# Optimization experiments

Measured on AMD Instinct MI355X. Metric: run time of the kernel, lower is better.

Reference implementation:

```python
import jax, jax.numpy as jnp
import numpy as np

LORA_ALPHA = 32
RANK = 16
TOP_K = 2
SCALING = LORA_ALPHA / RANK  # lora_alpha / r
EPS = 1e-9


def setup_inputs() -> dict:
    key = jax.random.key(0)
    ks = jax.random.split(key, 6)
    B, S, D_IN, D_OUT, E, R = 4, 2048, 4096, 4096, 8, RANK
    x = jax.random.normal(ks[0], (B, S, D_IN), dtype=jnp.float32)
    W = jax.random.normal(ks[1], (D_OUT, D_IN), dtype=jnp.float32) * (1.0 / np.sqrt(D_IN))
    bias = jax.random.normal(ks[2], (D_OUT,), dtype=jnp.float32) * 0.02
    route_W = jax.random.normal(ks[3], (E, D_IN), dtype=jnp.float32) * (1.0 / np.sqrt(D_IN))
    lora_A = jax.random.normal(ks[4], (E, R, D_IN), dtype=jnp.float32) * (1.0 / np.sqrt(D_IN))
    lora_B = jax.random.normal(ks[5], (D_OUT, R), dtype=jnp.float32)
    lora_B = jnp.broadcast_to(lora_B, (E, D_OUT, R)) * 0.01  # small nonzero so lora path matters
    return {"x": x, "W": W, "bias": bias, "route_W": route_W,
            "lora_A": lora_A, "lora_B": jnp.asarray(lora_B)}


def reference(x, W, bias, route_W, lora_A, lora_B):
    # Base dense projection: y = x W^T + b   [B,S,out]
    base = jnp.einsum('bsi,oi->bso', x, W) + bias

    # Router: softmax over experts in fp32, then top-k gating
    gate_score = jnp.einsum('bsi,ei->bse', x, route_W)          # [B,S,E]
    probs = jax.nn.softmax(gate_score.astype(jnp.float32), axis=-1)
    topk_vals, topk_idx = jax.lax.top_k(probs, TOP_K)           # [B,S,k]
    # renorm (top_k < lora_nums)
    topk_vals = topk_vals / (jnp.sum(topk_vals, axis=-1, keepdims=True) + EPS)
    # dense routing weights: zeros with top-k values scattered back  [B,S,E]
    E = probs.shape[-1]
    routing_weight = jnp.sum(
        jax.nn.one_hot(topk_idx, E, dtype=base.dtype) * topk_vals[..., None].astype(base.dtype),
        axis=-2)

    # Expert LoRA: identical math to the gather/index_add loop, expressed as
    # a dense weighted combine (weights are exactly 0 for unrouted experts).
    xf = x.astype(jnp.float32)
    h = jnp.einsum('bsi,eri->bser', xf, lora_A.astype(jnp.float32))      # [B,S,E,r] (small)
    hw = h * routing_weight.astype(jnp.float32)[..., None]               # gate per expert
    lora_out = jnp.einsum('bser,eor->bso', hw, lora_B.astype(jnp.float32))

    result = base + lora_out.astype(base.dtype) * SCALING
    return result, routing_weight, gate_score
```

## Files before the change

### kernel.cpp

```cpp
#include <hip/hip_runtime.h>
#include <hip/hip_bf16.h>

typedef __bf16 bf16_t;
typedef __bf16 bf16x8 __attribute__((ext_vector_type(8)));
typedef float floatx4 __attribute__((ext_vector_type(4)));

#define M_TOK 8192
#define K_DIM 4096
#define N_OUT 4096
#define NEXP  8
#define LRANK 16
#define KEXT  128
#define SCALING 2.0f

#define GLOAD_LDS16(g, l) \
    __builtin_amdgcn_global_load_lds((const __attribute__((address_space(1))) void*)(g), \
                                     (__attribute__((address_space(3))) void*)(l), 16, 0, 0)


__device__ __forceinline__ void pack4(bf16_t* dst, float4 v) {
    union { bf16_t h[4]; uint2 u; } t;
    t.h[0] = (bf16_t)v.x; t.h[1] = (bf16_t)v.y;
    t.h[2] = (bf16_t)v.z; t.h[3] = (bf16_t)v.w;
    *(uint2*)dst = t.u;
}

__device__ __forceinline__ void cvt8_body(const float* __restrict__ src,
                                          bf16_t* __restrict__ dst, int blk) {
    size_t i = (size_t)blk * 256 + threadIdx.x;
    float4 a = ((const float4*)src)[i * 2];
    float4 b = ((const float4*)src)[i * 2 + 1];
    union { bf16_t h[8]; uint4 u; } t;
    t.h[0] = (bf16_t)a.x; t.h[1] = (bf16_t)a.y; t.h[2] = (bf16_t)a.z; t.h[3] = (bf16_t)a.w;
    t.h[4] = (bf16_t)b.x; t.h[5] = (bf16_t)b.y; t.h[6] = (bf16_t)b.z; t.h[7] = (bf16_t)b.w;
    ((uint4*)dst)[i] = t.u;
}


#define PREP_W_BLKS   8192
#define PREP_A_BLKS   256
#define PREP_B_BLKS   2048

__global__ __launch_bounds__(256) void prep_all(const float* __restrict__ W,
                                                const float* __restrict__ loraA,
                                                const float* __restrict__ loraB,
                                                bf16_t* __restrict__ Wb,
                                                bf16_t* __restrict__ aflat,
                                                bf16_t* __restrict__ bflat) {
    int b = blockIdx.x;
    if (b < PREP_W_BLKS) {
        cvt8_body(W, Wb, b);
    } else if (b < PREP_W_BLKS + PREP_A_BLKS) {
        cvt8_body(loraA, aflat, b - PREP_W_BLKS);
    } else {
        int g = (b - PREP_W_BLKS - PREP_A_BLKS) * 256 + threadIdx.x;
        int o = g >> 7, j = g & 127;
        int e = j >> 4, r = j & 15;
        bflat[g] = (bf16_t)loraB[((size_t)e * N_OUT + o) * LRANK + r];
    }
}


__global__ __launch_bounds__(256) void gate_cvt16(const float* __restrict__ x,
                                                  const float* __restrict__ routeW,
                                                  bf16_t* __restrict__ xb,
                                                  float* __restrict__ rw_out,
                                                  float* __restrict__ gate_out)
{
    __shared__ float rwT[NEXP][256];
    int tid = threadIdx.x, lane = tid & 63, wave = tid >> 6;
    int tl = lane >> 4, seg = lane & 15;
    int t = blockIdx.x * 16 + wave * 4 + tl;
    const float* xrow = x + (size_t)t * K_DIM;
    bf16_t* xbrow = xb + (size_t)t * K_DIM;

    float acc[NEXP];
    #pragma unroll
    for (int e = 0; e < NEXP; ++e) acc[e] = 0.f;

    int srow = tid >> 5, scol = (tid & 31) * 8;

    for (int kk = 0; kk < K_DIM / 256; ++kk) {
        {
            const float4* src = (const float4*)(routeW + (size_t)srow * K_DIM + kk * 256 + scol);
            float4 v0 = src[0], v1 = src[1];
            *(float4*)&rwT[srow][scol]     = v0;
            *(float4*)&rwT[srow][scol + 4] = v1;
        }
        __syncthreads();
        #pragma unroll
        for (int kc = 0; kc < 4; ++kc) {
            int kloc = kc * 64 + seg * 4;
            int k = kk * 256 + kloc;
            float4 xv = *(const float4*)(xrow + k);
            union { bf16_t h[4]; uint2 u; } cv;
            cv.h[0] = (bf16_t)xv.x; cv.h[1] = (bf16_t)xv.y;
            cv.h[2] = (bf16_t)xv.z; cv.h[3] = (bf16_t)xv.w;
            *(uint2*)(xbrow + k) = cv.u;
            #pragma unroll
            for (int e = 0; e < NEXP; ++e) {
                float4 wv = *(const float4*)&rwT[e][kloc];
                acc[e] += xv.x * wv.x + xv.y * wv.y + xv.z * wv.z + xv.w * wv.w;
            }
        }
        __syncthreads();
    }

    #pragma unroll
    for (int e = 0; e < NEXP; ++e) {
        acc[e] += __shfl_xor(acc[e], 1);
        acc[e] += __shfl_xor(acc[e], 2);
        acc[e] += __shfl_xor(acc[e], 4);
        acc[e] += __shfl_xor(acc[e], 8);
    }

    if (seg == 0) {
        float mx = acc[0];
        #pragma unroll
        for (int e = 1; e < NEXP; ++e) mx = fmaxf(mx, acc[e]);
        float p[NEXP], s = 0.f;
        #pragma unroll
        for (int e = 0; e < NEXP; ++e) { p[e] = expf(acc[e] - mx); s += p[e]; }
        float inv_s = 1.0f / s;
        #pragma unroll
        for (int e = 0; e < NEXP; ++e) p[e] *= inv_s;
        int i0 = 0;
        #pragma unroll
        for (int e = 1; e < NEXP; ++e) if (p[e] > p[i0]) i0 = e;
        int i1 = (i0 == 0) ? 1 : 0;
        #pragma unroll
        for (int e = 0; e < NEXP; ++e) { if (e == i0 || e == i1) continue; if (p[e] > p[i1]) i1 = e; }
        float v0 = p[i0], v1 = p[i1];
        float inv = 1.0f / (v0 + v1 + 1e-9f);
        float r[NEXP];
        #pragma unroll
        for (int e = 0; e < NEXP; ++e) r[e] = 0.f;
        r[i0] = v0 * inv; r[i1] = v1 * inv;
        #pragma unroll
        for (int e = 0; e < NEXP; ++e) {
            gate_out[(size_t)t * NEXP + e] = acc[e];
            rw_out[(size_t)t * NEXP + e]  = r[e];
        }
    }
}


__global__ __launch_bounds__(256) void h_kernel_v3(const bf16_t* __restrict__ xb,
                                                   const bf16_t* __restrict__ aflat,
                                                   const float* __restrict__ rw,
                                                   bf16_t* __restrict__ hw)
{
    __shared__ bf16_t As[4 * 32 * 32];
    __shared__ bf16_t Bs[4 * 128 * 32];
    int tid = threadIdx.x, lane = tid & 63, wave = tid >> 6;
    int lrow = lane & 15, lq = lane >> 4;
    int n0 = wave * 32;
    int m0 = blockIdx.x * 32;
    floatx4 acc[2][2] = {};

    const bf16_t* srcA[2];
    #pragma unroll
    for (int i = 0; i < 2; ++i) {
        int idx = i * 256 + tid;
        int ks = idx >> 7, r = (idx >> 2) & 31, cc2 = idx & 3;
        srcA[i] = xb + (size_t)(m0 + r) * K_DIM + ks * 32 + cc2 * 8;
    }
    const bf16_t* srcB[8];
    #pragma unroll
    for (int i = 0; i < 8; ++i) {
        int idx = i * 256 + tid;
        int ks = idx >> 9, r = (idx >> 2) & 127, cc2 = idx & 3;
        srcB[i] = aflat + (size_t)r * K_DIM + ks * 32 + cc2 * 8;
    }

    for (int k0 = 0; k0 < K_DIM; k0 += 128) {
        #pragma unroll
        for (int i = 0; i < 2; ++i)
            GLOAD_LDS16(srcA[i] + k0, (char*)As + (i * 256 + wave * 64) * 16);
        #pragma unroll
        for (int i = 0; i < 8; ++i)
            GLOAD_LDS16(srcB[i] + k0, (char*)Bs + (i * 256 + wave * 64) * 16);
        __syncthreads();
        #pragma unroll
        for (int ks = 0; ks < 4; ++ks) {
            bf16x8 af[2], bfr[2];
            #pragma unroll
            for (int mi = 0; mi < 2; ++mi)
                af[mi] = *(const bf16x8*)(As + ks * 1024 + (mi * 16 + lrow) * 32 + lq * 8);
            #pragma unroll
            for (int ni = 0; ni < 2; ++ni)
                bfr[ni] = *(const bf16x8*)(Bs + ks * 4096 + (n0 + ni * 16 + lrow) * 32 + lq * 8);
            #pragma unroll
            for (int mi = 0; mi < 2; ++mi)
                #pragma unroll
                for (int ni = 0; ni < 2; ++ni)
                    acc[mi][ni] = __builtin_amdgcn_mfma_f32_16x16x32_bf16(af[mi], bfr[ni], acc[mi][ni], 0, 0, 0);
        }
        __syncthreads();
    }
    #pragma unroll
    for (int mi = 0; mi < 2; ++mi)
        #pragma unroll
        for (int ni = 0; ni < 2; ++ni)
            #pragma unroll
            for (int reg = 0; reg < 4; ++reg) {
                int t = m0 + mi * 16 + lq * 4 + reg;
                int j = n0 + ni * 16 + lrow;
                float g = rw[(size_t)t * NEXP + (j >> 4)] * SCALING;
                hw[(size_t)t * KEXT + j] = (bf16_t)(acc[mi][ni][reg] * g);
            }
}


__global__ __launch_bounds__(256) void main_gemm_v2(const bf16_t* __restrict__ xb,
                                                    const bf16_t* __restrict__ Wb,
                                                    const float* __restrict__ bias,
                                                    const bf16_t* __restrict__ hw,
                                                    const bf16_t* __restrict__ bflat,
                                                    float* __restrict__ out)
{
    __shared__ bf16_t As[128 * 64];
    __shared__ bf16_t Bs[128 * 64];
    int tid = threadIdx.x, lane = tid & 63, wave = tid >> 6;
    int lrow = lane & 15, lq = lane >> 4;
    int wm = (wave >> 1) * 64, wn = (wave & 1) * 64;
    int tm = blockIdx.y * 128, tn = blockIdx.x * 128;
    floatx4 acc[4][4] = {};

    const bf16_t* srcA[4];
    const bf16_t* srcB[4];
    #pragma unroll
    for (int i = 0; i < 4; ++i) {
        int s = i * 256 + tid;
        int row = s >> 3;
        int lg = (s & 7) ^ (row & 7);
        srcA[i] = xb + (size_t)(tm + row) * K_DIM + lg * 8;
        srcB[i] = Wb + (size_t)(tn + row) * K_DIM + lg * 8;
    }

    int swz = lrow & 7;

    for (int k0 = 0; k0 < K_DIM; k0 += 64) {
        #pragma unroll
        for (int i = 0; i < 4; ++i) {
            GLOAD_LDS16(srcA[i] + k0, (char*)As + i * 4096 + wave * 1024);
            GLOAD_LDS16(srcB[i] + k0, (char*)Bs + i * 4096 + wave * 1024);
        }
        __syncthreads();
        #pragma unroll
        for (int ks = 0; ks < 2; ++ks) {
            int go = ((ks * 4 + lq) ^ swz) * 8;
            bf16x8 af[4], bfr[4];
            #pragma unroll
            for (int mi = 0; mi < 4; ++mi)
                af[mi] = *(const bf16x8*)(As + (wm + mi * 16 + lrow) * 64 + go);
            #pragma unroll
            for (int ni = 0; ni < 4; ++ni)
                bfr[ni] = *(const bf16x8*)(Bs + (wn + ni * 16 + lrow) * 64 + go);
            #pragma unroll
            for (int mi = 0; mi < 4; ++mi)
                #pragma unroll
                for (int ni = 0; ni < 4; ++ni)
                    acc[mi][ni] = __builtin_amdgcn_mfma_f32_16x16x32_bf16(af[mi], bfr[ni], acc[mi][ni], 0, 0, 0);
        }
        __syncthreads();
    }

    {
        const bf16_t* eA[4];
        const bf16_t* eB[4];
        #pragma unroll
        for (int i = 0; i < 4; ++i) {
            int s = i * 256 + tid;
            int row = s >> 3;
            int lg = (s & 7) ^ (row & 7);
            eA[i] = hw    + (size_t)(tm + row) * KEXT + lg * 8;
            eB[i] = bflat + (size_t)(tn + row) * KEXT + lg * 8;
        }
        for (int k0 = 0; k0 < KEXT; k0 += 64) {
            #pragma unroll
            for (int i = 0; i < 4; ++i) {
                GLOAD_LDS16(eA[i] + k0, (char*)As + i * 4096 + wave * 1024);
                GLOAD_LDS16(eB[i] + k0, (char*)Bs + i * 4096 + wave * 1024);
            }
            __syncthreads();
            #pragma unroll
            for (int ks = 0; ks < 2; ++ks) {
                int go = ((ks * 4 + lq) ^ swz) * 8;
                bf16x8 af[4], bfr[4];
                #pragma unroll
                for (int mi = 0; mi < 4; ++mi)
                    af[mi] = *(const bf16x8*)(As + (wm + mi * 16 + lrow) * 64 + go);
                #pragma unroll
                for (int ni = 0; ni < 4; ++ni)
                    bfr[ni] = *(const bf16x8*)(Bs + (wn + ni * 16 + lrow) * 64 + go);
                #pragma unroll
                for (int mi = 0; mi < 4; ++mi)
                    #pragma unroll
                    for (int ni = 0; ni < 4; ++ni)
                        acc[mi][ni] = __builtin_amdgcn_mfma_f32_16x16x32_bf16(af[mi], bfr[ni], acc[mi][ni], 0, 0, 0);
            }
            __syncthreads();
        }
    }

    #pragma unroll
    for (int mi = 0; mi < 4; ++mi)
        #pragma unroll
        for (int ni = 0; ni < 4; ++ni) {
            int row = tm + wm + mi * 16 + lq * 4;
            int col = tn + wn + ni * 16 + lrow;
            float b = bias[col];
            #pragma unroll
            for (int reg = 0; reg < 4; ++reg)
                out[(size_t)(row + reg) * N_OUT + col] = acc[mi][ni][reg] + b;
        }
}


__global__ __launch_bounds__(256) void prep_bflat(const float* __restrict__ loraB,
                                                  bf16_t* __restrict__ bflat) {
    int g = blockIdx.x * 256 + threadIdx.x;
    int o = g >> 7, j = g & 127;
    int e = j >> 4, r = j & 15;
    bflat[g] = (bf16_t)loraB[((size_t)e * N_OUT + o) * LRANK + r];
}

__global__ __launch_bounds__(256) void gate_kernel(const float* __restrict__ x,
                                                   const float* __restrict__ routeW,
                                                   float* __restrict__ rw_out,
                                                   float* __restrict__ gate_out)
{
    int wave = threadIdx.x >> 6;
    int lane = threadIdx.x & 63;
    int t = blockIdx.x * 4 + wave;
    const float4* xp = (const float4*)(x + (size_t)t * K_DIM);
    float acc[NEXP];
    #pragma unroll
    for (int e = 0; e < NEXP; ++e) acc[e] = 0.f;
    #pragma unroll 4
    for (int it = 0; it < K_DIM / 256; ++it) {
        float4 xv = xp[it * 64 + lane];
        #pragma unroll
        for (int e = 0; e < NEXP; ++e) {
            float4 wv = ((const float4*)(routeW + (size_t)e * K_DIM))[it * 64 + lane];
            acc[e] += xv.x * wv.x + xv.y * wv.y + xv.z * wv.z + xv.w * wv.w;
        }
    }
    #pragma unroll
    for (int e = 0; e < NEXP; ++e)
        for (int off = 32; off > 0; off >>= 1)
            acc[e] += __shfl_xor(acc[e], off, 64);
    if (lane == 0) {
        float mx = acc[0];
        #pragma unroll
        for (int e = 1; e < NEXP; ++e) mx = fmaxf(mx, acc[e]);
        float p[NEXP], s = 0.f;
        #pragma unroll
        for (int e = 0; e < NEXP; ++e) { p[e] = expf(acc[e] - mx); s += p[e]; }
        float inv_s = 1.0f / s;
        #pragma unroll
        for (int e = 0; e < NEXP; ++e) p[e] *= inv_s;
        int i0 = 0;
        #pragma unroll
        for (int e = 1; e < NEXP; ++e) if (p[e] > p[i0]) i0 = e;
        int i1 = (i0 == 0) ? 1 : 0;
        #pragma unroll
        for (int e = 0; e < NEXP; ++e) { if (e == i0 || e == i1) continue; if (p[e] > p[i1]) i1 = e; }
        float v0 = p[i0], v1 = p[i1];
        float inv = 1.0f / (v0 + v1 + 1e-9f);
        float r[NEXP];
        #pragma unroll
        for (int e = 0; e < NEXP; ++e) r[e] = 0.f;
        r[i0] = v0 * inv; r[i1] = v1 * inv;
        #pragma unroll
        for (int e = 0; e < NEXP; ++e) {
            gate_out[(size_t)t * NEXP + e] = acc[e];
            rw_out[(size_t)t * NEXP + e]  = r[e];
        }
    }
}

__global__ __launch_bounds__(256) void h_kernel(const float* __restrict__ x,
                                                const float* __restrict__ loraA,
                                                const float* __restrict__ rw,
                                                bf16_t* __restrict__ hw)
{
    __shared__ bf16_t As[32][40];
    __shared__ bf16_t Bs[128][40];
    int tid = threadIdx.x;
    int wave = tid >> 6, lane = tid & 63;
    int lrow = lane & 15, lq = lane >> 4;
    int m0 = blockIdx.x * 32;
    floatx4 acc[2][2] = {};
    int rb = tid >> 1, cb = (tid & 1) * 16;
    for (int k0 = 0; k0 < K_DIM; k0 += 32) {
        if (tid < 64) {
            const float* srcA = x + (size_t)(m0 + rb) * K_DIM + k0 + cb;
            #pragma unroll
            for (int q = 0; q < 4; ++q) pack4(&As[rb][cb + q * 4], ((const float4*)srcA)[q]);
        }
        {
            const float* srcB = loraA + (size_t)rb * K_DIM + k0 + cb;
            #pragma unroll
            for (int q = 0; q < 4; ++q) pack4(&Bs[rb][cb + q * 4], ((const float4*)srcB)[q]);
        }
        __syncthreads();
        bf16x8 af[2], bfr[2];
        #pragma unroll
        for (int mi = 0; mi < 2; ++mi) af[mi] = *(const bf16x8*)&As[mi * 16 + lrow][lq * 8];
        #pragma unroll
        for (int ni = 0; ni < 2; ++ni) bfr[ni] = *(const bf16x8*)&Bs[wave * 32 + ni * 16 + lrow][lq * 8];
        #pragma unroll
        for (int mi = 0; mi < 2; ++mi)
            #pragma unroll
            for (int ni = 0; ni < 2; ++ni)
                acc[mi][ni] = __builtin_amdgcn_mfma_f32_16x16x32_bf16(af[mi], bfr[ni], acc[mi][ni], 0, 0, 0);
        __syncthreads();
    }
    #pragma unroll
    for (int mi = 0; mi < 2; ++mi)
        #pragma unroll
        for (int ni = 0; ni < 2; ++ni)
            #pragma unroll
            for (int reg = 0; reg < 4; ++reg) {
                int t = m0 + mi * 16 + lq * 4 + reg;
                int j = wave * 32 + ni * 16 + lrow;
                float g = rw[(size_t)t * NEXP + (j >> 4)] * SCALING;
                hw[(size_t)t * KEXT + j] = (bf16_t)(acc[mi][ni][reg] * g);
            }
}

__device__ __forceinline__ void mma_step(const bf16_t (*As)[40], const bf16_t (*Bs)[40],
                                         floatx4 acc[4][4], int wm, int wn, int lrow, int lq) {
    bf16x8 af[4], bfr[4];
    #pragma unroll
    for (int mi = 0; mi < 4; ++mi) af[mi] = *(const bf16x8*)&As[wm + mi * 16 + lrow][lq * 8];
    #pragma unroll
    for (int ni = 0; ni < 4; ++ni) bfr[ni] = *(const bf16x8*)&Bs[wn + ni * 16 + lrow][lq * 8];
    #pragma unroll
    for (int mi = 0; mi < 4; ++mi)
        #pragma unroll
        for (int ni = 0; ni < 4; ++ni)
            acc[mi][ni] = __builtin_amdgcn_mfma_f32_16x16x32_bf16(af[mi], bfr[ni], acc[mi][ni], 0, 0, 0);
}

__global__ __launch_bounds__(256) void main_gemm(const float* __restrict__ x,
                                                 const float* __restrict__ W,
                                                 const float* __restrict__ bias,
                                                 const bf16_t* __restrict__ hw,
                                                 const bf16_t* __restrict__ bflat,
                                                 float* __restrict__ out)
{
    __shared__ bf16_t As[128][40];
    __shared__ bf16_t Bs[128][40];
    int tid = threadIdx.x, lane = tid & 63, wave = tid >> 6;
    int lrow = lane & 15, lq = lane >> 4;
    int wm = (wave >> 1) * 64, wn = (wave & 1) * 64;
    int tm = blockIdx.y * 128, tn = blockIdx.x * 128;
    floatx4 acc[4][4] = {};
    int rb = tid >> 1, cb = (tid & 1) * 16;
    const float* gA = x + (size_t)(tm + rb) * K_DIM + cb;
    const float* gB = W + (size_t)(tn + rb) * K_DIM + cb;
    for (int k0 = 0; k0 < K_DIM; k0 += 32) {
        #pragma unroll
        for (int q = 0; q < 4; ++q) {
            pack4(&As[rb][cb + q * 4], ((const float4*)(gA + k0))[q]);
            pack4(&Bs[rb][cb + q * 4], ((const float4*)(gB + k0))[q]);
        }
        __syncthreads();
        mma_step(As, Bs, acc, wm, wn, lrow, lq);
        __syncthreads();
    }
    const bf16_t* eA = hw    + (size_t)(tm + rb) * KEXT + cb;
    const bf16_t* eB = bflat + (size_t)(tn + rb) * KEXT + cb;
    for (int k0 = 0; k0 < KEXT; k0 += 32) {
        *(uint4*)&As[rb][cb]     = *(const uint4*)(eA + k0);
        *(uint4*)&As[rb][cb + 8] = *(const uint4*)(eA + k0 + 8);
        *(uint4*)&Bs[rb][cb]     = *(const uint4*)(eB + k0);
        *(uint4*)&Bs[rb][cb + 8] = *(const uint4*)(eB + k0 + 8);
        __syncthreads();
        mma_step(As, Bs, acc, wm, wn, lrow, lq);
        __syncthreads();
    }
    #pragma unroll
    for (int mi = 0; mi < 4; ++mi)
        #pragma unroll
        for (int ni = 0; ni < 4; ++ni) {
            int row = tm + wm + mi * 16 + lq * 4;
            int col = tn + wn + ni * 16 + lrow;
            float b = bias[col];
            #pragma unroll
            for (int reg = 0; reg < 4; ++reg)
                out[(size_t)(row + reg) * N_OUT + col] = acc[mi][ni][reg] + b;
        }
}


extern "C" void kernel_launch(void* const* d_in, const int* in_sizes, int n_in,
                              void* d_out, int out_size, void* d_ws, size_t ws_size,
                              hipStream_t stream) {
    const float* x      = (const float*)d_in[0];
    const float* W      = (const float*)d_in[1];
    const float* bias   = (const float*)d_in[2];
    const float* routeW = (const float*)d_in[3];
    const float* loraA  = (const float*)d_in[4];
    const float* loraB  = (const float*)d_in[5];

    float* out0 = (float*)d_out;
    float* out1 = out0 + (size_t)M_TOK * N_OUT;
    float* out2 = out1 + (size_t)M_TOK * NEXP;

    size_t need = ((size_t)M_TOK * K_DIM + (size_t)N_OUT * K_DIM +
                   (size_t)KEXT * K_DIM + (size_t)N_OUT * KEXT +
                   (size_t)M_TOK * KEXT) * sizeof(bf16_t);

    if (ws_size >= need) {
        bf16_t* xb    = (bf16_t*)d_ws;
        bf16_t* Wb    = xb + (size_t)M_TOK * K_DIM;
        bf16_t* aflat = Wb + (size_t)N_OUT * K_DIM;
        bf16_t* bflat = aflat + (size_t)KEXT * K_DIM;
        bf16_t* hw    = bflat + (size_t)N_OUT * KEXT;

        hipLaunchKernelGGL(prep_all, dim3(PREP_W_BLKS + PREP_A_BLKS + PREP_B_BLKS), dim3(256), 0, stream,
                           W, loraA, loraB, Wb, aflat, bflat);
        hipLaunchKernelGGL(gate_cvt16, dim3(M_TOK / 16), dim3(256), 0, stream, x, routeW, xb, out1, out2);
        hipLaunchKernelGGL(h_kernel_v3, dim3(M_TOK / 32), dim3(256), 0, stream, xb, aflat, out1, hw);
        hipLaunchKernelGGL(main_gemm_v2, dim3(N_OUT / 128, M_TOK / 128), dim3(256), 0, stream,
                           xb, Wb, bias, hw, bflat, out0);
    } else {
        bf16_t* bflat = (bf16_t*)d_ws;
        bf16_t* hw    = bflat + (size_t)N_OUT * KEXT;
        hipLaunchKernelGGL(prep_bflat, dim3((N_OUT * KEXT) / 256), dim3(256), 0, stream, loraB, bflat);
        hipLaunchKernelGGL(gate_kernel, dim3(M_TOK / 4), dim3(256), 0, stream, x, routeW, out1, out2);
        hipLaunchKernelGGL(h_kernel, dim3(M_TOK / 32), dim3(256), 0, stream, x, loraA, out1, hw);
        hipLaunchKernelGGL(main_gemm, dim3(N_OUT / 128, M_TOK / 128), dim3(256), 0, stream,
                           x, W, bias, hw, bflat, out0);
    }
}
```

Measured before the change: 605.8 us.

## Fuse router gating, x bf16 conversion and LoRA-A projection into one kernel

Merges the gate/convert kernel and the LoRA h-projection kernel into a single kernel that reads fp32 x once. It converts x to bf16 for both the global copy and the LDS tile, accumulates router logits alongside the MFMA LoRA-A product, and applies the top-k routing weights from shared memory. This removes one launch and the re-read of xb from global memory. In exchange the K step shrinks to 64 with a plain synchronous x load per iteration, which may expose more latency and lower the number of gate blocks.

New measurement: 654.4 us. 8.0% more time.

```diff
diff --git a/kernel.cpp b/kernel.cpp
--- a/kernel.cpp
+++ b/kernel.cpp
@@ -61,135 +61,78 @@
 }
 
 
-__global__ __launch_bounds__(256) void gate_cvt16(const float* __restrict__ x,
-                                                  const float* __restrict__ routeW,
-                                                  bf16_t* __restrict__ xb,
-                                                  float* __restrict__ rw_out,
-                                                  float* __restrict__ gate_out)
+__global__ __launch_bounds__(256) void gate_h_fused(const float* __restrict__ x,
+                                                    const float* __restrict__ routeW,
+                                                    const bf16_t* __restrict__ aflat,
+                                                    bf16_t* __restrict__ xb,
+                                                    float* __restrict__ rw_out,
+                                                    float* __restrict__ gate_out,
+                                                    bf16_t* __restrict__ hw)
 {
-    __shared__ float rwT[NEXP][256];
-    int tid = threadIdx.x, lane = tid & 63, wave = tid >> 6;
-    int tl = lane >> 4, seg = lane & 15;
-    int t = blockIdx.x * 16 + wave * 4 + tl;
-    const float* xrow = x + (size_t)t * K_DIM;
-    bf16_t* xbrow = xb + (size_t)t * K_DIM;
-
-    float acc[NEXP];
-    #pragma unroll
-    for (int e = 0; e < NEXP; ++e) acc[e] = 0.f;
-
-    int srow = tid >> 5, scol = (tid & 31) * 8;
-
-    for (int kk = 0; kk < K_DIM / 256; ++kk) {
-        {
-            const float4* src = (const float4*)(routeW + (size_t)srow * K_DIM + kk * 256 + scol);
-            float4 v0 = src[0], v1 = src[1];
-            *(float4*)&rwT[srow][scol]     = v0;
-            *(float4*)&rwT[srow][scol + 4] = v1;
-        }
-        __syncthreads();
-        #pragma unroll
-        for (int kc = 0; kc < 4; ++kc) {
-            int kloc = kc * 64 + seg * 4;
-            int k = kk * 256 + kloc;
-            float4 xv = *(const float4*)(xrow + k);
-            union { bf16_t h[4]; uint2 u; } cv;
-            cv.h[0] = (bf16_t)xv.x; cv.h[1] = (bf16_t)xv.y;
-            cv.h[2] = (bf16_t)xv.z; cv.h[3] = (bf16_t)xv.w;
-            *(uint2*)(xbrow + k) = cv.u;
-            #pragma unroll
-            for (int e = 0; e < NEXP; ++e) {
-                float4 wv = *(const float4*)&rwT[e][kloc];
-                acc[e] += xv.x * wv.x + xv.y * wv.y + xv.z * wv.z + xv.w * wv.w;
-            }
-        }
-        __syncthreads();
-    }
-
-    #pragma unroll
-    for (int e = 0; e < NEXP; ++e) {
-        acc[e] += __shfl_xor(acc[e], 1);
-        acc[e] += __shfl_xor(acc[e], 2);
-        acc[e] += __shfl_xor(acc[e], 4);
-        acc[e] += __shfl_xor(acc[e], 8);
-    }
-
-    if (seg == 0) {
-        float mx = acc[0];
-        #pragma unroll
-        for (int e = 1; e < NEXP; ++e) mx = fmaxf(mx, acc[e]);
-        float p[NEXP], s = 0.f;
-        #pragma unroll
-        for (int e = 0; e < NEXP; ++e) { p[e] = expf(acc[e] - mx); s += p[e]; }
-        float inv_s = 1.0f / s;
-        #pragma unroll
-        for (int e = 0; e < NEXP; ++e) p[e] *= inv_s;
-        int i0 = 0;
-        #pragma unroll
-        for (int e = 1; e < NEXP; ++e) if (p[e] > p[i0]) i0 = e;
-        int i1 = (i0 == 0) ? 1 : 0;
-        #pragma unroll
-        for (int e = 0; e < NEXP; ++e) { if (e == i0 || e == i1) continue; if (p[e] > p[i1]) i1 = e; }
-        float v0 = p[i0], v1 = p[i1];
-        float inv = 1.0f / (v0 + v1 + 1e-9f);
-        float r[NEXP];
-        #pragma unroll
-        for (int e = 0; e < NEXP; ++e) r[e] = 0.f;
-        r[i0] = v0 * inv; r[i1] = v1 * inv;
-        #pragma unroll
-        for (int e = 0; e < NEXP; ++e) {
-            gate_out[(size_t)t * NEXP + e] = acc[e];
-            rw_out[(size_t)t * NEXP + e]  = r[e];
-        }
-    }
-}
-
-
-__global__ __launch_bounds__(256) void h_kernel_v3(const bf16_t* __restrict__ xb,
-                                                   const bf16_t* __restrict__ aflat,
-                                                   const float* __restrict__ rw,
-                                                   bf16_t* __restrict__ hw)
-{
-    __shared__ bf16_t As[4 * 32 * 32];
-    __shared__ bf16_t Bs[4 * 128 * 32];
+    __shared__ bf16_t As[32 * 64];
+    __shared__ bf16_t Bs[128 * 64];
+    __shared__ float rwT[NEXP][64];
+    __shared__ float rwS[32][NEXP];
+
     int tid = threadIdx.x, lane = tid & 63, wave = tid >> 6;
     int lrow = lane & 15, lq = lane >> 4;
     int n0 = wave * 32;
     int m0 = blockIdx.x * 32;
+    int r = tid >> 3, s = tid & 7;
+
     floatx4 acc[2][2] = {};
-
-    const bf16_t* srcA[2];
-    #pragma unroll
-    for (int i = 0; i < 2; ++i) {
-        int idx = i * 256 + tid;
-        int ks = idx >> 7, r = (idx >> 2) & 31, cc2 = idx & 3;
-        srcA[i] = xb + (size_t)(m0 + r) * K_DIM + ks * 32 + cc2 * 8;
-    }
-    const bf16_t* srcB[8];
-    #pragma unroll
-    for (int i = 0; i < 8; ++i) {
-        int idx = i * 256 + tid;
-        int ks = idx >> 9, r = (idx >> 2) & 127, cc2 = idx & 3;
-        srcB[i] = aflat + (size_t)r * K_DIM + ks * 32 + cc2 * 8;
-    }
-
-    for (int k0 = 0; k0 < K_DIM; k0 += 128) {
-        #pragma unroll
-        for (int i = 0; i < 2; ++i)
-            GLOAD_LDS16(srcA[i] + k0, (char*)As + (i * 256 + wave * 64) * 16);
-        #pragma unroll
-        for (int i = 0; i < 8; ++i)
-            GLOAD_LDS16(srcB[i] + k0, (char*)Bs + (i * 256 + wave * 64) * 16);
-        __syncthreads();
-        #pragma unroll
-        for (int ks = 0; ks < 4; ++ks) {
+    float g_acc[NEXP];
+    #pragma unroll
+    for (int e = 0; e < NEXP; ++e) g_acc[e] = 0.f;
+
+    const float* xsrc = x  + (size_t)(m0 + r) * K_DIM + s * 8;
+    bf16_t*      xdst = xb + (size_t)(m0 + r) * K_DIM + s * 8;
+    bf16_t*      aw   = As + r * 64 + (s ^ (r & 7)) * 8;
+
+    const bf16_t* srcB[4];
+    #pragma unroll
+    for (int i = 0; i < 4; ++i) {
+        int sl = i * 256 + tid;
+        int row = sl >> 3, g = sl & 7;
+        srcB[i] = aflat + (size_t)row * K_DIM + (g ^ (row & 7)) * 8;
+    }
+    int swz = lrow & 7;
+
+    for (int k0 = 0; k0 < K_DIM; k0 += 64) {
+        #pragma unroll
+        for (int i = 0; i < 4; ++i)
+            GLOAD_LDS16(srcB[i] + k0, (char*)Bs + i * 4096 + wave * 1024);
+        if (tid < 128) {
+            int er = tid >> 4, c4 = (tid & 15) * 4;
+            *(float4*)&rwT[er][c4] = *(const float4*)(routeW + (size_t)er * K_DIM + k0 + c4);
+        }
+        float4 xa = *(const float4*)(xsrc + k0);
+        float4 xbv = *(const float4*)(xsrc + k0 + 4);
+        union { bf16_t h[8]; uint4 u; } cv;
+        cv.h[0] = (bf16_t)xa.x;  cv.h[1] = (bf16_t)xa.y;
+        cv.h[2] = (bf16_t)xa.z;  cv.h[3] = (bf16_t)xa.w;
+        cv.h[4] = (bf16_t)xbv.x; cv.h[5] = (bf16_t)xbv.y;
+        cv.h[6] = (bf16_t)xbv.z; cv.h[7] = (bf16_t)xbv.w;
+        *(uint4*)(xdst + k0) = cv.u;
+        *(uint4*)aw = cv.u;
+        __syncthreads();
+        #pragma unroll
+        for (int e = 0; e < NEXP; ++e) {
+            float4 wa = *(const float4*)&rwT[e][s * 8];
+            float4 wb = *(const float4*)&rwT[e][s * 8 + 4];
+            g_acc[e] += xa.x * wa.x + xa.y * wa.y + xa.z * wa.z + xa.w * wa.w
+                      + xbv.x * wb.x + xbv.y * wb.y + xbv.z * wb.z + xbv.w * wb.w;
+        }
+        #pragma unroll
+        for (int ks = 0; ks < 2; ++ks) {
+            int go = ((ks * 4 + lq) ^ swz) * 8;
             bf16x8 af[2], bfr[2];
             #pragma unroll
             for (int mi = 0; mi < 2; ++mi)
-                af[mi] = *(const bf16x8*)(As + ks * 1024 + (mi * 16 + lrow) * 32 + lq * 8);
+                af[mi] = *(const bf16x8*)(As + (mi * 16 + lrow) * 64 + go);
             #pragma unroll
             for (int ni = 0; ni < 2; ++ni)
-                bfr[ni] = *(const bf16x8*)(Bs + ks * 4096 + (n0 + ni * 16 + lrow) * 32 + lq * 8);
+                bfr[ni] = *(const bf16x8*)(Bs + (n0 + ni * 16 + lrow) * 64 + go);
             #pragma unroll
             for (int mi = 0; mi < 2; ++mi)
                 #pragma unroll
@@ -198,16 +141,56 @@
         }
         __syncthreads();
     }
+
+    #pragma unroll
+    for (int e = 0; e < NEXP; ++e) {
+        g_acc[e] += __shfl_xor(g_acc[e], 1);
+        g_acc[e] += __shfl_xor(g_acc[e], 2);
+        g_acc[e] += __shfl_xor(g_acc[e], 4);
+    }
+
+    if (s == 0) {
+        int t = m0 + r;
+        float mx = g_acc[0];
+        #pragma unroll
+        for (int e = 1; e < NEXP; ++e) mx = fmaxf(mx, g_acc[e]);
+        float p[NEXP], sum = 0.f;
+        #pragma unroll
+        for (int e = 0; e < NEXP; ++e) { p[e] = expf(g_acc[e] - mx); sum += p[e]; }
+        float inv_s = 1.0f / sum;
+        #pragma unroll
+        for (int e = 0; e < NEXP; ++e) p[e] *= inv_s;
+        int i0 = 0;
+        #pragma unroll
+        for (int e = 1; e < NEXP; ++e) if (p[e] > p[i0]) i0 = e;
+        int i1 = (i0 == 0) ? 1 : 0;
+        #pragma unroll
+        for (int e = 0; e < NEXP; ++e) { if (e == i0 || e == i1) continue; if (p[e] > p[i1]) i1 = e; }
+        float v0 = p[i0], v1 = p[i1];
+        float inv = 1.0f / (v0 + v1 + 1e-9f);
+        float rr[NEXP];
+        #pragma unroll
+        for (int e = 0; e < NEXP; ++e) rr[e] = 0.f;
+        rr[i0] = v0 * inv; rr[i1] = v1 * inv;
+        #pragma unroll
+        for (int e = 0; e < NEXP; ++e) {
+            gate_out[(size_t)t * NEXP + e] = g_acc[e];
+            rw_out[(size_t)t * NEXP + e]  = rr[e];
+            rwS[r][e] = rr[e];
+        }
+    }
+    __syncthreads();
+
     #pragma unroll
     for (int mi = 0; mi < 2; ++mi)
         #pragma unroll
         for (int ni = 0; ni < 2; ++ni)
             #pragma unroll
             for (int reg = 0; reg < 4; ++reg) {
-                int t = m0 + mi * 16 + lq * 4 + reg;
-                int j = n0 + ni * 16 + lrow;
-                float g = rw[(size_t)t * NEXP + (j >> 4)] * SCALING;
-                hw[(size_t)t * KEXT + j] = (bf16_t)(acc[mi][ni][reg] * g);
+                int lr = mi * 16 + lq * 4 + reg;
+                int j  = n0 + ni * 16 + lrow;
+                float g = rwS[lr][j >> 4] * SCALING;
+                hw[(size_t)(m0 + lr) * KEXT + j] = (bf16_t)(acc[mi][ni][reg] * g);
             }
 }
 
@@ -237,7 +220,6 @@
         srcA[i] = xb + (size_t)(tm + row) * K_DIM + lg * 8;
         srcB[i] = Wb + (size_t)(tn + row) * K_DIM + lg * 8;
     }
-
     int swz = lrow & 7;
 
     for (int k0 = 0; k0 < K_DIM; k0 += 64) {
@@ -524,8 +506,8 @@
 
         hipLaunchKernelGGL(prep_all, dim3(PREP_W_BLKS + PREP_A_BLKS + PREP_B_BLKS), dim3(256), 0, stream,
                            W, loraA, loraB, Wb, aflat, bflat);
-        hipLaunchKernelGGL(gate_cvt16, dim3(M_TOK / 16), dim3(256), 0, stream, x, routeW, xb, out1, out2);
-        hipLaunchKernelGGL(h_kernel_v3, dim3(M_TOK / 32), dim3(256), 0, stream, xb, aflat, out1, hw);
+        hipLaunchKernelGGL(gate_h_fused, dim3(M_TOK / 32), dim3(256), 0, stream,
+                           x, routeW, aflat, xb, out1, out2, hw);
         hipLaunchKernelGGL(main_gemm_v2, dim3(N_OUT / 128, M_TOK / 128), dim3(256), 0, stream,
                            xb, Wb, bias, hw, bflat, out0);
     } else {
```
